# Performance work log

Hardware: AMD Instinct MI355X
Metric: run time of the kernel (lower is better)

The kernel has to match this reference:

```python
import jax, jax.numpy as jnp
import numpy as np

B, T, D, V = 32, 384, 768, 32000
PAD = 1
THRESH = 0.95

def setup_inputs() -> dict:
    key = jax.random.key(0)
    ks = jax.random.split(key, 8)
    s = 1.0 / np.sqrt(D)
    sentence = jax.random.randint(ks[0], (B, T), 0, V)
    emb = jax.random.normal(ks[1], (V, D), jnp.float32) * 0.02
    emb = emb.at[PAD].set(0.0)  # padding_idx row is zero
    w_ih = jax.random.uniform(ks[2], (3 * D, D), jnp.float32, -s, s)
    w_hh = jax.random.uniform(ks[3], (3 * D, D), jnp.float32, -s, s)
    b_ih = jax.random.uniform(ks[4], (3 * D,), jnp.float32, -s, s)
    b_hh = jax.random.uniform(ks[5], (3 * D,), jnp.float32, -s, s)
    w_act = jax.random.uniform(ks[6], (D,), jnp.float32, -s, s)
    b_act = jnp.zeros((1,), jnp.float32)
    return dict(sentence=sentence, emb=emb, w_ih=w_ih, w_hh=w_hh,
                b_ih=b_ih, b_hh=b_hh, w_act=w_act, b_act=b_act)


def _gru(x, w_ih, w_hh, b_ih, b_hh):
    # x: [B,T,D] -> states [B,T,D]; PyTorch GRU cell math.
    xp = jnp.einsum('btd,ed->bte', x, w_ih) + b_ih  # [B,T,3D]

    def step(h, xt):
        hp = h @ w_hh.T + b_hh
        xr, xz, xn = jnp.split(xt, 3, axis=-1)
        hr, hz, hn = jnp.split(hp, 3, axis=-1)
        r = jax.nn.sigmoid(xr + hr)
        z = jax.nn.sigmoid(xz + hz)
        n = jnp.tanh(xn + r * hn)
        h_new = (1.0 - z) * n + z * h
        return h_new, h_new

    h0 = jnp.zeros((x.shape[0], w_hh.shape[1]), x.dtype)
    _, hs = jax.lax.scan(step, h0, jnp.swapaxes(xp, 0, 1))
    return jnp.swapaxes(hs, 0, 1)


def _forward(sentence, emb, w_ih, w_hh, b_ih, b_hh, w_act, b_act):
    x = emb[sentence]                                   # [B,T,D]
    states = _gru(x, w_ih, w_hh, b_ih, b_hh)            # [B,T,D]
    probs = jax.nn.sigmoid(states @ w_act + b_act)      # [B,T]

    # ACT-style halting: accumulate probs, emit a segment when sum > threshold.
    def halt_step(hsum, p):
        acc = hsum + p
        halted = acc > THRESH
        return jnp.where(halted, 0.0, acc), halted

    _, halted_t = jax.lax.scan(halt_step, jnp.zeros((B,), probs.dtype), probs.T)
    halted = halted_t.T                                 # [B,T] bool, True at last step of each segment
    h_i = halted.astype(jnp.int32)
    seg_id = jnp.cumsum(h_i, axis=1) - h_i              # exclusive cumsum: segment index per step

    segsum = jax.vmap(lambda v, s: jax.ops.segment_sum(v, s, num_segments=T))
    sum_p = segsum(probs, seg_id)                       # [B,T] per-segment prob sum
    sum_p_at = jnp.take_along_axis(sum_p, seg_id, axis=1)
    # last step of a segment gets weight p_last - stopgrad(sum_seg - 1)
    weights = jnp.where(halted, probs - jax.lax.stop_gradient(sum_p_at - 1.0), probs)
    seg_embs = segsum(states * weights[..., None], seg_id)  # [B,T,D]

    n_segs = h_i.sum(axis=1)                            # [B] completed segments
    valid = jnp.arange(T)[None, :] < n_segs[:, None]    # [B,T]
    embs = jnp.where(valid[..., None], seg_embs, 0.0)   # zero-pad incomplete slots
    embs = embs.reshape(B * T, D)                       # concat padded per-batch lists
    return embs, probs[..., None]


def reference(sentence, emb, w_ih, w_hh, b_ih, b_hh, w_act, b_act):
    return _forward(sentence, emb, w_ih, w_hh, b_ih, b_hh, w_act, b_act)
```

## Files before the change

### kernel.cpp

```cpp
#include <hip/hip_runtime.h>
#include <math.h>

#define BATCH 32
#define SEQT 384
#define DIM 768
#define D3 2304
#define NROWS (BATCH*SEQT)
#define VTHRESH 0.95f

typedef float  f32x4 __attribute__((ext_vector_type(4)));

#define OFF_XP   ((size_t)0)
#define SZ_XP    ((size_t)NROWS * D3 * 4)
#define OFF_ST   (OFF_XP + SZ_XP)
#define SZ_ST    ((size_t)NROWS * DIM * 4)
#define OFF_PR   (OFF_ST + SZ_ST)
#define SZ_PR    ((size_t)NROWS * 4)
#define OFF_WT   (OFF_PR + SZ_PR)
#define OFF_SS   (OFF_WT + SZ_PR)
#define OFF_SE   (OFF_SS + SZ_PR)
#define OFF_NS   (OFF_SE + SZ_PR)
#define OFF_HB   (OFF_NS + 256)
#define NBG 8
#define BPG 4
#define WPB 32
#define CPW 24
#define BGBYTES ((size_t)(DIM * 2 * 16))
#define SZ_HB   ((size_t)2 * NBG * BGBYTES)
#define INIT_FLOATS (SZ_HB/4)

#define DOT4(a,b) ((a).x*(b).x + (a).y*(b).y + (a).z*(b).z + (a).w*(b).w)

__device__ __forceinline__ float fexp2(float x) {
    float r; asm("v_exp_f32 %0, %1" : "=v"(r) : "v"(x)); return r;
}
__device__ __forceinline__ float frcp(float x) {
    float r; asm("v_rcp_f32 %0, %1" : "=v"(r) : "v"(x)); return r;
}
#define LOG2E 1.44269504f

__global__ __launch_bounds__(256, 2) void k_xp(
    const int* __restrict__ sent, const float* __restrict__ emb,
    const float* __restrict__ w_ih, const float* __restrict__ b_ih,
    float* __restrict__ xp)
{
    __shared__ float As[16][132];
    __shared__ float Bs[16][132];
    const int tid = threadIdx.x;
    const int mt = blockIdx.x, nt = blockIdx.y;
    const int tx = tid & 15, ty = tid >> 4;
    const int lm = tid >> 2;
    const int lk = (tid & 3) << 2;

    const long arow0 = (long)sent[mt*128 + lm] * DIM;
    const long arow1 = (long)sent[mt*128 + lm + 64] * DIM;
    const float* b0p = w_ih + (size_t)(nt*128 + lm) * DIM;
    const float* b1p = w_ih + (size_t)(nt*128 + lm + 64) * DIM;

    float acc[8][8];
    #pragma unroll
    for (int i = 0; i < 8; ++i)
        #pragma unroll
        for (int j = 0; j < 8; ++j) acc[i][j] = 0.f;

    for (int k0 = 0; k0 < DIM; k0 += 16) {
        float4 a0 = *(const float4*)(emb + arow0 + k0 + lk);
        float4 a1 = *(const float4*)(emb + arow1 + k0 + lk);
        float4 b0 = *(const float4*)(b0p + k0 + lk);
        float4 b1 = *(const float4*)(b1p + k0 + lk);
        __syncthreads();
        As[lk+0][lm] = a0.x; As[lk+1][lm] = a0.y; As[lk+2][lm] = a0.z; As[lk+3][lm] = a0.w;
        As[lk+0][lm+64] = a1.x; As[lk+1][lm+64] = a1.y; As[lk+2][lm+64] = a1.z; As[lk+3][lm+64] = a1.w;
        Bs[lk+0][lm] = b0.x; Bs[lk+1][lm] = b0.y; Bs[lk+2][lm] = b0.z; Bs[lk+3][lm] = b0.w;
        Bs[lk+0][lm+64] = b1.x; Bs[lk+1][lm+64] = b1.y; Bs[lk+2][lm+64] = b1.z; Bs[lk+3][lm+64] = b1.w;
        __syncthreads();
        #pragma unroll
        for (int k = 0; k < 16; ++k) {
            float4 av0 = *(const float4*)&As[k][ty*8];
            float4 av1 = *(const float4*)&As[k][ty*8+4];
            float4 bv0 = *(const float4*)&Bs[k][tx*8];
            float4 bv1 = *(const float4*)&Bs[k][tx*8+4];
            float a[8] = {av0.x,av0.y,av0.z,av0.w,av1.x,av1.y,av1.z,av1.w};
            float b[8] = {bv0.x,bv0.y,bv0.z,bv0.w,bv1.x,bv1.y,bv1.z,bv1.w};
            #pragma unroll
            for (int i = 0; i < 8; ++i)
                #pragma unroll
                for (int j = 0; j < 8; ++j)
                    acc[i][j] += a[i]*b[j];
        }
    }

    const int m0 = mt*128 + ty*8;
    const int n0 = nt*128 + tx*8;
    float4 bi0 = *(const float4*)(b_ih + n0);
    float4 bi1 = *(const float4*)(b_ih + n0 + 4);
    #pragma unroll
    for (int i = 0; i < 8; ++i) {
        float4 v0, v1;
        v0.x = acc[i][0] + bi0.x; v0.y = acc[i][1] + bi0.y;
        v0.z = acc[i][2] + bi0.z; v0.w = acc[i][3] + bi0.w;
        v1.x = acc[i][4] + bi1.x; v1.y = acc[i][5] + bi1.y;
        v1.z = acc[i][6] + bi1.z; v1.w = acc[i][7] + bi1.w;
        *(float4*)(xp + (size_t)(m0+i)*D3 + n0)     = v0;
        *(float4*)(xp + (size_t)(m0+i)*D3 + n0 + 4) = v1;
    }
}

#define HPITCH 772

__global__ __launch_bounds__(768, 1) void k_gru(
    const float* __restrict__ w_hh, const float* __restrict__ b_hh,
    const float* __restrict__ xp, float* __restrict__ states,
    char* __restrict__ hbuf)
{
    __shared__ float h_lds[2][BPG][HPITCH];

    const int tid = threadIdx.x;
    const int jb  = blockIdx.x & 31;
    const int bg  = blockIdx.x >> 5;
    const int w    = tid >> 6;
    const int lane = tid & 63;
    const int half = lane >> 5;
    const int c32  = lane & 31;
    const int col  = jb*CPW + w*2 + half;
    const int bloc = (c32 >> 3) & 3;
    const int batch = bg*BPG + bloc;

    f32x4 w4[3][6];
    #pragma unroll
    for (int g3 = 0; g3 < 3; ++g3) {
        const float* wr = w_hh + (size_t)(g3*DIM + col)*DIM + c32*4;
        #pragma unroll
        for (int m = 0; m < 6; ++m) {
            const f32x4* ap = (const f32x4*)(wr + m*128);
            asm volatile("global_load_dwordx4 %0, %1, off"
                         : "=v"(w4[g3][m]) : "v"(ap));
        }
    }
    asm volatile("s_waitcnt vmcnt(0)" ::: "memory");
    __builtin_amdgcn_sched_barrier(0);

    const float bhr = b_hh[col];
    const float bhz = b_hh[DIM + col];
    const float bhn = b_hh[2*DIM + col];

    int goff[2], ldsoff[2], onemask = 0;
    #pragma unroll
    for (int i = 0; i < 2; ++i) {
        int q = i*768 + tid;
        int cq = q >> 1, sq = q & 1;
        goff[i]   = q << 4;
        ldsoff[i] = (sq ? 3 : 0)*HPITCH + cq;
        if (sq) onemask |= (1<<i);
    }

    char* pb[2];
    pb[0] = hbuf + (size_t)(0*NBG + bg)*BGBYTES;
    pb[1] = hbuf + (size_t)(1*NBG + bg)*BGBYTES;

    const float* xq = xp + (size_t)batch*SEQT*D3 + col;

    f32x4 ch[2];

#define ISSUE_POLLS(pbx)                                                 \
    {                                                                    \
        _Pragma("unroll")                                                \
        for (int k = 0; k < 2; ++k) {                                    \
            const f32x4* ap = (const f32x4*)((pbx) + goff[k]);           \
            asm volatile("global_load_dwordx4 %0, %1, off sc0 sc1"       \
                         : "=v"(ch[k]) : "v"(ap));                       \
        }                                                                \
    }

#define GRU_GATES(xr, xz, xn, ar, az, an)                                \
    {                                                                    \
        float rg = frcp(1.f + fexp2(-LOG2E*((xr) + (ar) + bhr)));        \
        float zg = frcp(1.f + fexp2(-LOG2E*((xz) + (az) + bhz)));        \
        float sn = (xn) + rg * ((an) + bhn);                             \
        float ng = 1.f - 2.f*frcp(1.f + fexp2(2.f*LOG2E*sn));            \
        hold = (1.f - zg) * ng + zg * hold;                              \
    }

#define PUBLISH(pbx, tt)                                                 \
    {                                                                    \
        int gp = (lane >> 1) & 1;                                        \
        int sq = lane & 1;                                               \
        float q0 = __shfl(hold, gp*32 + (sq ? 24 : 0));                  \
        float q1 = __shfl(hold, gp*32 + 8);                              \
        float q2 = __shfl(hold, gp*32 + 16);                             \
        if (lane < 4) {                                                  \
            f32x4 val;                                                   \
            val.x = q0; val.y = q1; val.z = q2;                          \
            val.w = __int_as_float((tt) + 1);                            \
            int colp = jb*CPW + w*2 + gp;                                \
            f32x4* ap = (f32x4*)((pbx) + (size_t)(colp*2 + sq)*16);      \
            asm volatile("global_store_dwordx4 %0, %1, off sc0 sc1"      \
                         :: "v"(ap), "v"(val) : "memory");               \
        }                                                                \
        if ((c32 & 7) == 0)                                              \
            states[(size_t)(batch*SEQT + (tt))*DIM + col] = hold;        \
    }

    float hold = 0.f;

    float xr = xq[0], xz = xq[DIM], xn = xq[2*DIM];
    GRU_GATES(xr, xz, xn, 0.f, 0.f, 0.f);
    PUBLISH(pb[0], 0);
    ISSUE_POLLS(pb[0]);
    float xrn = xq[(size_t)D3], xzn = xq[(size_t)D3 + DIM],
          xnn = xq[(size_t)D3 + 2*DIM];

    for (int t = 1; t < SEQT; ++t) {
        float* hb0 = &h_lds[t & 1][0][0];
        const char* pbx = pb[(t-1)&1];

        asm volatile("s_waitcnt vmcnt(0)" ::: "memory");
        __builtin_amdgcn_sched_barrier(0);
        bool up_ok = (__float_as_int(ch[1].w) == t);
        while (__float_as_int(ch[0].w) != t) {
            __builtin_amdgcn_s_sleep(1);
            {
                const f32x4* a0 = (const f32x4*)(pbx + goff[0]);
                asm volatile("global_load_dwordx4 %0, %1, off sc0 sc1"
                             : "=v"(ch[0]) : "v"(a0));
            }
            if (!up_ok) {
                const f32x4* a1 = (const f32x4*)(pbx + goff[1]);
                asm volatile("global_load_dwordx4 %0, %1, off sc0 sc1"
                             : "=v"(ch[1]) : "v"(a1));
            }
            asm volatile("s_waitcnt vmcnt(0)" ::: "memory");
            __builtin_amdgcn_sched_barrier(0);
            if (!up_ok) up_ok = (__float_as_int(ch[1].w) == t);
        }
        hb0[ldsoff[0]] = ch[0].x;
        if (!(onemask & 1)) {
            hb0[ldsoff[0] + HPITCH]   = ch[0].y;
            hb0[ldsoff[0] + 2*HPITCH] = ch[0].z;
        }
        if (up_ok) {
            hb0[ldsoff[1]] = ch[1].x;
            if (!(onemask & 2)) {
                hb0[ldsoff[1] + HPITCH]   = ch[1].y;
                hb0[ldsoff[1] + 2*HPITCH] = ch[1].z;
            }
        } else {
            const f32x4* a1 = (const f32x4*)(pbx + goff[1]);
            asm volatile("global_load_dwordx4 %0, %1, off sc0 sc1"
                         : "=v"(ch[1]) : "v"(a1));
        }
        xr = xrn; xz = xzn; xn = xnn;
        __syncthreads();

        float v[12];
        #pragma unroll
        for (int i = 0; i < 12; ++i) v[i] = 0.f;
        const float* hk = hb0 + c32*4;
        #pragma unroll
        for (int bb = 0; bb < 4; ++bb) {
            const float* hr = hk + bb*HPITCH;
            #pragma unroll
            for (int m = 0; m < 3; ++m) {
                f32x4 h4 = *(const f32x4*)(hr + m*128);
                v[bb*3+0] += DOT4(h4, w4[0][m]);
                v[bb*3+1] += DOT4(h4, w4[1][m]);
                v[bb*3+2] += DOT4(h4, w4[2][m]);
            }
        }

        if (!up_ok) {
            asm volatile("s_waitcnt vmcnt(0)" ::: "memory");
            __builtin_amdgcn_sched_barrier(0);
            while (__float_as_int(ch[1].w) != t) {
                __builtin_amdgcn_s_sleep(1);
                const f32x4* a1 = (const f32x4*)(pbx + goff[1]);
                asm volatile("global_load_dwordx4 %0, %1, off sc0 sc1"
                             : "=v"(ch[1]) : "v"(a1));
                asm volatile("s_waitcnt vmcnt(0)" ::: "memory");
                __builtin_amdgcn_sched_barrier(0);
            }
            hb0[ldsoff[1]] = ch[1].x;
            if (!(onemask & 2)) {
                hb0[ldsoff[1] + HPITCH]   = ch[1].y;
                hb0[ldsoff[1] + 2*HPITCH] = ch[1].z;
            }
        }
        __syncthreads();

        if (t + 1 < SEQT) {
            xrn = xq[(size_t)(t+1)*D3];
            xzn = xq[(size_t)(t+1)*D3 + DIM];
            xnn = xq[(size_t)(t+1)*D3 + 2*DIM];
        }

        #pragma unroll
        for (int bb = 0; bb < 4; ++bb) {
            const float* hr = hk + bb*HPITCH;
            #pragma unroll
            for (int m = 3; m < 6; ++m) {
                f32x4 h4 = *(const f32x4*)(hr + m*128);
                v[bb*3+0] += DOT4(h4, w4[0][m]);
                v[bb*3+1] += DOT4(h4, w4[1][m]);
                v[bb*3+2] += DOT4(h4, w4[2][m]);
            }
        }
        #pragma unroll
        for (int i = 0; i < 6; ++i) {
            float send = (c32 & 16) ? v[i] : v[i+6];
            float keep = (c32 & 16) ? v[i+6] : v[i];
            v[i] = keep + __shfl_xor(send, 16);
        }
        #pragma unroll
        for (int i = 0; i < 3; ++i) {
            float send = (c32 & 8) ? v[i] : v[i+3];
            float keep = (c32 & 8) ? v[i+3] : v[i];
            v[i] = keep + __shfl_xor(send, 8);
        }
        #pragma unroll
        for (int i = 0; i < 3; ++i) v[i] += __shfl_xor(v[i], 4);
        #pragma unroll
        for (int i = 0; i < 3; ++i) v[i] += __shfl_xor(v[i], 2);
        #pragma unroll
        for (int i = 0; i < 3; ++i) v[i] += __shfl_xor(v[i], 1);

        GRU_GATES(xr, xz, xn, v[0], v[1], v[2]);
        PUBLISH(pb[t&1], t);
        if (t + 1 < SEQT)
            ISSUE_POLLS(pb[t&1]);
    }
#undef ISSUE_POLLS
#undef GRU_GATES
#undef PUBLISH
}

__global__ __launch_bounds__(256, 4) void k_probs(
    const float* __restrict__ states, const float* __restrict__ w_act,
    const float* __restrict__ b_act, float* __restrict__ probs,
    float* __restrict__ out_probs)
{
    int row  = blockIdx.x*4 + (threadIdx.x >> 6);
    int lane = threadIdx.x & 63;
    const float* sr = states + (size_t)row * DIM;
    float s = 0.f;
    #pragma unroll
    for (int i = 0; i < 3; ++i) {
        float4 v = *(const float4*)(sr + i*256 + lane*4);
        float4 w = *(const float4*)(w_act + i*256 + lane*4);
        s += v.x*w.x + v.y*w.y + v.z*w.z + v.w*w.w;
    }
    #pragma unroll
    for (int off = 32; off > 0; off >>= 1) s += __shfl_xor(s, off);
    if (lane == 0) {
        float pv = 1.f / (1.f + expf(-(s + b_act[0])));
        probs[row]     = pv;
        out_probs[row] = pv;
    }
}

__global__ void k_scan(const float* __restrict__ probs, float* __restrict__ weights,
                       int* __restrict__ seg_start, int* __restrict__ seg_end,
                       int* __restrict__ n_segs)
{
    int b = threadIdx.x;
    if (b >= BATCH) return;
    float acc = 0.f;
    int s = 0, start = 0;
    for (int t0 = 0; t0 < SEQT; t0 += 4) {
        float4 p4 = *(const float4*)(probs + b*SEQT + t0);
        float pv[4] = {p4.x, p4.y, p4.z, p4.w};
        #pragma unroll
        for (int k = 0; k < 4; ++k) {
            int t = t0 + k;
            float pp = pv[k];
            acc += pp;
            float w = pp;
            if (acc > VTHRESH) {
                w = pp - (acc - 1.0f);
                seg_start[b*SEQT + s] = start;
                seg_end[b*SEQT + s]   = t;
                s++; start = t + 1; acc = 0.f;
            }
            weights[b*SEQT + t] = w;
        }
    }
    n_segs[b] = s;
}

__global__ __launch_bounds__(256, 4) void k_embs(
    const float* __restrict__ states, const float* __restrict__ weights,
    const int* __restrict__ seg_start, const int* __restrict__ seg_end,
    const int* __restrict__ n_segs, float* __restrict__ out)
{
    int r = blockIdx.x;
    int b = r / SEQT;
    int s = r - b*SEQT;
    int tid = threadIdx.x;
    float a0 = 0.f, a1 = 0.f, a2 = 0.f;
    if (s < n_segs[b]) {
        int st = seg_start[r], en = seg_end[r];
        for (int t = st; t <= en; ++t) {
            float w = weights[b*SEQT + t];
            const float* sp = states + (size_t)(b*SEQT + t) * DIM;
            a0 += w * sp[tid];
            a1 += w * sp[tid + 256];
            a2 += w * sp[tid + 512];
        }
    }
    float* o = out + (size_t)r * DIM;
    o[tid]       = a0;
    o[tid + 256] = a1;
    o[tid + 512] = a2;
}

__global__ void k_init(float* hb) {
    int i = blockIdx.x * 256 + threadIdx.x;
    if (i < INIT_FLOATS) hb[i] = 0.f;
}

extern "C" void kernel_launch(void* const* d_in, const int* in_sizes, int n_in,
                              void* d_out, int out_size, void* d_ws, size_t ws_size,
                              hipStream_t stream)
{
    const int*   sent  = (const int*)d_in[0];
    const float* emb   = (const float*)d_in[1];
    const float* w_ih  = (const float*)d_in[2];
    const float* w_hh  = (const float*)d_in[3];
    const float* b_ih  = (const float*)d_in[4];
    const float* b_hh  = (const float*)d_in[5];
    const float* w_act = (const float*)d_in[6];
    const float* b_act = (const float*)d_in[7];
    float* out = (float*)d_out;

    char* ws = (char*)d_ws;
    float* xp      = (float*)(ws + OFF_XP);
    float* states  = (float*)(ws + OFF_ST);
    float* probs   = (float*)(ws + OFF_PR);
    float* weights = (float*)(ws + OFF_WT);
    int*   sstart  = (int*)(ws + OFF_SS);
    int*   send    = (int*)(ws + OFF_SE);
    int*   nsegs   = (int*)(ws + OFF_NS);
    char*  hbuf    = (char*)(ws + OFF_HB);

    k_init<<<384, 256, 0, stream>>>((float*)hbuf);
    k_xp<<<dim3(96, 18), 256, 0, stream>>>(sent, emb, w_ih, b_ih, xp);
    k_gru<<<256, 768, 0, stream>>>(w_hh, b_hh, xp, states, hbuf);
    k_probs<<<NROWS/4, 256, 0, stream>>>(states, w_act, b_act, probs,
                                         out + (size_t)NROWS * DIM);
    k_scan<<<1, 64, 0, stream>>>(probs, weights, sstart, send, nsegs);
    k_embs<<<NROWS, 256, 0, stream>>>(states, weights, sstart, send, nsegs, out);
}
```

Baseline: 2.197 ms.

## Remap GRU block indices and poll peer state with lighter cache-scope loads

Block-to-work mapping is swapped so consecutive blocks take different batch groups instead of different column slices, which changes which blocks share a polling group and possibly their placement across XCDs. Most cross-block polling loads now use sc0 only instead of sc0 sc1, with a full sc0 sc1 load every fourth spin. The aim is cheaper, lower-latency spin polling on the recurrent step barrier. The risk is that sc0-only loads can hit stale cached lines when the peer block sits on another XCD, so the wait may not see the published step until a periodic full-scope load runs, which can stretch the latency.

Measured after the change: 2.647 ms. 1.2x slower.

```diff
diff --git a/kernel.cpp b/kernel.cpp
--- a/kernel.cpp
+++ b/kernel.cpp
@@ -116,8 +116,8 @@
     __shared__ float h_lds[2][BPG][HPITCH];
 
     const int tid = threadIdx.x;
-    const int jb  = blockIdx.x & 31;
-    const int bg  = blockIdx.x >> 5;
+    const int jb  = blockIdx.x >> 3;
+    const int bg  = blockIdx.x & 7;
     const int w    = tid >> 6;
     const int lane = tid & 63;
     const int half = lane >> 5;
@@ -162,14 +162,23 @@
 
     f32x4 ch[2];
 
+#define LOADCH_FAST(idx, pbx)                                            \
+    {                                                                    \
+        const f32x4* ap = (const f32x4*)((pbx) + goff[idx]);             \
+        asm volatile("global_load_dwordx4 %0, %1, off sc0"               \
+                     : "=v"(ch[idx]) : "v"(ap));                         \
+    }
+#define LOADCH_SLOW(idx, pbx)                                            \
+    {                                                                    \
+        const f32x4* ap = (const f32x4*)((pbx) + goff[idx]);             \
+        asm volatile("global_load_dwordx4 %0, %1, off sc0 sc1"           \
+                     : "=v"(ch[idx]) : "v"(ap));                         \
+    }
+
 #define ISSUE_POLLS(pbx)                                                 \
     {                                                                    \
-        _Pragma("unroll")                                                \
-        for (int k = 0; k < 2; ++k) {                                    \
-            const f32x4* ap = (const f32x4*)((pbx) + goff[k]);           \
-            asm volatile("global_load_dwordx4 %0, %1, off sc0 sc1"       \
-                         : "=v"(ch[k]) : "v"(ap));                       \
-        }                                                                \
+        LOADCH_FAST(0, pbx);                                             \
+        LOADCH_FAST(1, pbx);                                             \
     }
 
 #define GRU_GATES(xr, xz, xn, ar, az, an)                                \
@@ -217,21 +226,22 @@
         asm volatile("s_waitcnt vmcnt(0)" ::: "memory");
         __builtin_amdgcn_sched_barrier(0);
         bool up_ok = (__float_as_int(ch[1].w) == t);
-        while (__float_as_int(ch[0].w) != t) {
-            __builtin_amdgcn_s_sleep(1);
-            {
-                const f32x4* a0 = (const f32x4*)(pbx + goff[0]);
-                asm volatile("global_load_dwordx4 %0, %1, off sc0 sc1"
-                             : "=v"(ch[0]) : "v"(a0));
-            }
-            if (!up_ok) {
-                const f32x4* a1 = (const f32x4*)(pbx + goff[1]);
-                asm volatile("global_load_dwordx4 %0, %1, off sc0 sc1"
-                             : "=v"(ch[1]) : "v"(a1));
-            }
-            asm volatile("s_waitcnt vmcnt(0)" ::: "memory");
-            __builtin_amdgcn_sched_barrier(0);
-            if (!up_ok) up_ok = (__float_as_int(ch[1].w) == t);
+        {
+            int spin = 0;
+            while (__float_as_int(ch[0].w) != t) {
+                __builtin_amdgcn_s_sleep(1);
+                ++spin;
+                if ((spin & 3) == 0) {
+                    LOADCH_SLOW(0, pbx);
+                    if (!up_ok) LOADCH_SLOW(1, pbx);
+                } else {
+                    LOADCH_FAST(0, pbx);
+                    if (!up_ok) LOADCH_FAST(1, pbx);
+                }
+                asm volatile("s_waitcnt vmcnt(0)" ::: "memory");
+                __builtin_amdgcn_sched_barrier(0);
+                if (!up_ok) up_ok = (__float_as_int(ch[1].w) == t);
+            }
         }
         hb0[ldsoff[0]] = ch[0].x;
         if (!(onemask & 1)) {
@@ -245,9 +255,7 @@
                 hb0[ldsoff[1] + 2*HPITCH] = ch[1].z;
             }
         } else {
-            const f32x4* a1 = (const f32x4*)(pbx + goff[1]);
-            asm volatile("global_load_dwordx4 %0, %1, off sc0 sc1"
-                         : "=v"(ch[1]) : "v"(a1));
+            LOADCH_FAST(1, pbx);
         }
         xr = xrn; xz = xzn; xn = xnn;
         __syncthreads();
@@ -271,11 +279,12 @@
         if (!up_ok) {
             asm volatile("s_waitcnt vmcnt(0)" ::: "memory");
             __builtin_amdgcn_sched_barrier(0);
+            int spin = 0;
             while (__float_as_int(ch[1].w) != t) {
                 __builtin_amdgcn_s_sleep(1);
-                const f32x4* a1 = (const f32x4*)(pbx + goff[1]);
-                asm volatile("global_load_dwordx4 %0, %1, off sc0 sc1"
-                             : "=v"(ch[1]) : "v"(a1));
+                ++spin;
+                if ((spin & 3) == 0) { LOADCH_SLOW(1, pbx); }
+                else                 { LOADCH_FAST(1, pbx); }
                 asm volatile("s_waitcnt vmcnt(0)" ::: "memory");
                 __builtin_amdgcn_sched_barrier(0);
             }
@@ -329,6 +338,8 @@
             ISSUE_POLLS(pb[t&1]);
     }
 #undef ISSUE_POLLS
+#undef LOADCH_FAST
+#undef LOADCH_SLOW
 #undef GRU_GATES
 #undef PUBLISH
 }
```
